# Kernel optimization log

Hardware: AMD Instinct MI355X
Metric: run time of the kernel (lower is better)

The kernel has to match this reference:

```python
import jax, jax.numpy as jnp
import numpy as np

DIM = 768
H = 12
HD = DIM // H  # 64
B = 16
N = 1025  # cls token + 1024 patches; RoPE applied to tokens 1:


def setup_inputs() -> dict:
    key = jax.random.key(0)
    k1, k2, k3, k4, k5, k6 = jax.random.split(key, 6)
    x = jax.random.normal(k1, (B, N, DIM), dtype=jnp.float32)
    # rotary angles for the N-1 non-cls tokens, HD//2 freq pairs
    theta = jax.random.uniform(k2, (N - 1, HD // 2), dtype=jnp.float32) * 2.0 * jnp.pi
    freqs_cos = jnp.cos(theta)
    freqs_sin = jnp.sin(theta)
    W_qkv = jax.random.normal(k3, (3 * DIM, DIM), dtype=jnp.float32) * 0.02
    W_proj = jax.random.normal(k4, (DIM, DIM), dtype=jnp.float32) * 0.02
    b_proj = jax.random.normal(k5, (DIM,), dtype=jnp.float32) * 0.02
    return {"x": x, "freqs_cos": freqs_cos, "freqs_sin": freqs_sin,
            "W_qkv": W_qkv, "W_proj": W_proj, "b_proj": b_proj}


def _apply_rope(t, cos, sin):
    # t: [b, h, m, d]; cos/sin: [m, d/2]. Pairs are interleaved (even, odd),
    # matching torch.view_as_complex on a (..., d/2, 2) reshape.
    tr = t[..., 0::2]
    ti = t[..., 1::2]
    cos = cos[None, None, :, :]
    sin = sin[None, None, :, :]
    out_r = tr * cos - ti * sin
    out_i = tr * sin + ti * cos
    # interleave back: (..., d/2, 2) -> (..., d)
    out = jnp.stack([out_r, out_i], axis=-1)
    return out.reshape(t.shape)


def reference(x, freqs_cos, freqs_sin, W_qkv, W_proj, b_proj):
    b, n, dim = x.shape
    h, hd = H, HD
    scale = hd ** -0.5

    qkv = jnp.einsum('bnd,ed->bne', x, W_qkv)            # [b, n, 3*dim]
    qkv = qkv.reshape(b, n, 3, h, hd)
    q = jnp.transpose(qkv[:, :, 0], (0, 2, 1, 3))         # [b, h, n, hd]
    k = jnp.transpose(qkv[:, :, 1], (0, 2, 1, 3))
    v = jnp.transpose(qkv[:, :, 2], (0, 2, 1, 3))

    # RoPE on all tokens except the cls token (index 0)
    q = jnp.concatenate([q[:, :, :1], _apply_rope(q[:, :, 1:], freqs_cos, freqs_sin)], axis=2)
    k = jnp.concatenate([k[:, :, :1], _apply_rope(k[:, :, 1:], freqs_cos, freqs_sin)], axis=2)

    dots = jnp.einsum('bhid,bhjd->bhij', q, k) * scale    # [b, h, n, n]
    attn = jax.nn.softmax(dots, axis=-1)
    out = jnp.einsum('bhij,bhjd->bhid', attn, v)          # [b, h, n, hd]
    out = jnp.transpose(out, (0, 2, 1, 3)).reshape(b, n, dim)
    out = jnp.einsum('bnd,ed->bne', out, W_proj) + b_proj
    return out
```

## Files before the change

kernel.cpp:

```cpp
#include <hip/hip_runtime.h>
#include <stdint.h>

#define NH 12
#define HD64 64
#define SEQ 1025
#define M_ROWS (16 * SEQ)
#define DIM 768
#define NPAD 1088

typedef __attribute__((ext_vector_type(8))) short bf16x8;
typedef __attribute__((ext_vector_type(4))) float f32x4;
typedef __attribute__((ext_vector_type(4))) short s16x4;

#define VMCNT(n) asm volatile("s_waitcnt vmcnt(" #n ")" ::: "memory")

__device__ __forceinline__ short f2bf_rne(float f) {
    union { float f; uint32_t u; } c; c.f = f;
    uint32_t u = c.u + 0x7fffu + ((c.u >> 16) & 1u);
    return (short)(u >> 16);
}

__device__ __forceinline__ int cvt_pk_bf16(float lo, float hi) {
    int r;
    asm("v_cvt_pk_bf16_f32 %0, %1, %2" : "=v"(r) : "v"(lo), "v"(hi));
    return r;
}

__device__ __forceinline__ void gload_lds16(const void* g, void* l) {
    __builtin_amdgcn_global_load_lds(
        (const __attribute__((address_space(1))) void*)g,
        (__attribute__((address_space(3))) void*)l, 16, 0, 0);
}

__device__ __forceinline__ int xcd_chunk_swizzle(int orig, int nwg) {
    int q = nwg >> 3, r = nwg & 7;
    int xcd = orig & 7, i = orig >> 3;
    int start = (xcd < r) ? xcd * (q + 1) : r * (q + 1) + (xcd - r) * q;
    return start + i;
}

__global__ void f2bf3_kernel(const float* __restrict__ a, short* __restrict__ ao, int na4,
                             const float* __restrict__ b, short* __restrict__ bo, int nb4,
                             const float* __restrict__ c, short* __restrict__ co, int nc4) {
    int i = blockIdx.x * blockDim.x + threadIdx.x;
    const float* src; short* dst; int idx;
    if (i < na4) { src = a; dst = ao; idx = i; }
    else if (i < na4 + nb4) { src = b; dst = bo; idx = i - na4; }
    else if (i < na4 + nb4 + nc4) { src = c; dst = co; idx = i - na4 - nb4; }
    else return;
    f32x4 f = ((const f32x4*)src)[idx];
    s16x4 o;
    o[0] = f2bf_rne(f[0]); o[1] = f2bf_rne(f[1]);
    o[2] = f2bf_rne(f[2]); o[3] = f2bf_rne(f[3]);
    ((s16x4*)dst)[idx] = o;
}


__global__ __launch_bounds__(512) void qkv_gemm_kernel(
    const short* __restrict__ xb, const short* __restrict__ wb,
    const float* __restrict__ fcos, const float* __restrict__ fsin,
    short* __restrict__ Qb, short* __restrict__ Kb, short* __restrict__ VTb)
{
    __shared__ short Alds[4][256 * 32];
    __shared__ short Blds[4][256 * 32];
    const int tid = threadIdx.x;
    const int lane = tid & 63, w = tid >> 6;
    const int wm = w >> 2, wn = w & 3;
    const int lr = lane & 15, lg = lane >> 4;
    const int tile = xcd_chunk_swizzle(blockIdx.x, 65 * 9);
    const int mt = tile / 9, nt = tile - (tile / 9) * 9;

    const int c0 = tid, c1 = tid + 512;
    int ra0 = mt * 256 + (c0 >> 2); if (ra0 > M_ROWS - 1) ra0 = M_ROWS - 1;
    int ra1 = mt * 256 + (c1 >> 2); if (ra1 > M_ROWS - 1) ra1 = M_ROWS - 1;
    const int g0 = (c0 & 3) ^ ((c0 >> 2) & 3) ^ ((c0 >> 4) & 1);
    const int g1 = (c1 & 3) ^ ((c1 >> 2) & 3) ^ ((c1 >> 4) & 1);
    const short* gA0 = xb + (size_t)ra0 * DIM + g0 * 8;
    const short* gA1 = xb + (size_t)ra1 * DIM + g1 * 8;
    const short* gB0 = wb + (size_t)(nt * 256 + (c0 >> 2)) * DIM + g0 * 8;
    const short* gB1 = wb + (size_t)(nt * 256 + (c1 >> 2)) * DIM + g1 * 8;
    short* lA0 = &Alds[0][0] + c0 * 8;
    short* lA1 = &Alds[0][0] + c1 * 8;
    short* lB0 = &Blds[0][0] + c0 * 8;
    short* lB1 = &Blds[0][0] + c1 * 8;

    auto stage = [&](int buf, int kt) {
        const int ko = kt * 32;
        const int lo = buf * (256 * 32);
        gload_lds16(gA0 + ko, lA0 + lo);
        gload_lds16(gA1 + ko, lA1 + lo);
        gload_lds16(gB0 + ko, lB0 + lo);
        gload_lds16(gB1 + ko, lB1 + lo);
    };

    f32x4 acc[8][4];
#pragma unroll
    for (int i = 0; i < 8; i++)
#pragma unroll
        for (int j = 0; j < 4; j++) acc[i][j] = (f32x4)0.0f;

    stage(0, 0); stage(1, 1); stage(2, 2);

    const int ablk = (lg ^ (lr & 3) ^ ((lr >> 2) & 1)) * 8;

    for (int t = 0; t < 24; ++t) {
        if (t < 22) { VMCNT(8); } else if (t == 22) { VMCNT(4); } else { VMCNT(0); }
        __builtin_amdgcn_s_barrier();

        const short* Ab = &Alds[0][0] + (t & 3) * (256 * 32);
        const short* Bb = &Blds[0][0] + (t & 3) * (256 * 32);

        if (t < 21) stage((t + 3) & 3, t + 3);

        bf16x8 bF[4], aF[8];
#pragma unroll
        for (int ni = 0; ni < 4; ni++)
            bF[ni] = *(const bf16x8*)&Bb[(wn * 64 + ni * 16 + lr) * 32 + ablk];
#pragma unroll
        for (int mi = 0; mi < 8; mi++)
            aF[mi] = *(const bf16x8*)&Ab[(wm * 128 + mi * 16 + lr) * 32 + ablk];

        __builtin_amdgcn_s_setprio(1);
#pragma unroll
        for (int mi = 0; mi < 8; mi++)
#pragma unroll
            for (int ni = 0; ni < 4; ni++)
                acc[mi][ni] = __builtin_amdgcn_mfma_f32_16x16x32_bf16(aF[mi], bF[ni], acc[mi][ni], 0, 0, 0);
        __builtin_amdgcn_s_setprio(0);
    }

#pragma unroll
    for (int mi = 0; mi < 8; mi++) {
        int mbase = mt * 256 + wm * 128 + mi * 16 + lg * 4;
#pragma unroll
        for (int j = 0; j < 4; j++) {
            int m = mbase + j;
            bool valid = (m < M_ROWS);
            int mm = valid ? m : 0;
            int b = mm / SEQ;
            int n = mm - b * SEQ;
#pragma unroll
            for (int ni = 0; ni < 4; ni++) {
                int e = nt * 256 + wn * 64 + ni * 16 + lr;
                int qkv = e / DIM;
                int rem = e - qkv * DIM;
                int h = rem >> 6, d = rem & 63;
                float v = acc[mi][ni][j];
                float vo = __shfl_xor(v, 1);
                float outv = v;
                if (qkv < 2 && n > 0) {
                    float cs = fcos[(n - 1) * 32 + (d >> 1)];
                    float sn = fsin[(n - 1) * 32 + (d >> 1)];
                    outv = (d & 1) ? (vo * sn + v * cs) : (v * cs - vo * sn);
                }
                if (qkv == 0) outv *= 0.180336881f;
                if (valid) {
                    short bv = f2bf_rne(outv);
                    size_t bh = (size_t)b * NH + h;
                    if (qkv == 0)      Qb[(bh * SEQ + n) * HD64 + d] = bv;
                    else if (qkv == 1) Kb[(bh * SEQ + n) * HD64 + d] = bv;
                    else               VTb[(bh * HD64 + d) * NPAD + n] = bv;
                }
            }
        }
    }
}

__global__ __launch_bounds__(256) void attn_kernel(
    const short* __restrict__ Qb, const short* __restrict__ Kb,
    const short* __restrict__ VTb, short* __restrict__ AO)
{
    __shared__ short Klds[2][64 * 64];
    __shared__ short Vlds[2][64 * 64];
    __shared__ int Plds[4][16 * 32];
    const int tid = threadIdx.x;
    const int lane = tid & 63, w = tid >> 6;
    const int lr = lane & 15, lg = lane >> 4;
    const int tile = xcd_chunk_swizzle(blockIdx.x, 17 * 192);
    const int bh = tile / 17, qt = tile - (tile / 17) * 17;
    const int b = bh / NH, h = bh - b * NH;

    const short* Qp = Qb + (size_t)bh * SEQ * HD64;
    const short* Kp = Kb + (size_t)bh * SEQ * HD64;
    const short* Vp = VTb + (size_t)bh * HD64 * NPAD;

    int qr = qt * 64 + w * 16 + lr; if (qr > SEQ - 1) qr = SEQ - 1;
    bf16x8 qf0 = *(const bf16x8*)&Qp[(size_t)qr * HD64 + 0 + lg * 8];
    bf16x8 qf1 = *(const bf16x8*)&Qp[(size_t)qr * HD64 + 32 + lg * 8];

    float m_i = -1e30f, l_i = 0.f;
    f32x4 acc[4];
#pragma unroll
    for (int vt = 0; vt < 4; vt++) acc[vt] = (f32x4)0.0f;

    int* pw = &Plds[w][0];
    const int pswz = (lr & 3) << 3;

    auto stageKV = [&](int buf, int t) {
        int k0 = t * 64;
#pragma unroll
        for (int i = 0; i < 2; i++) {
            int c = i * 256 + tid;
            int row = c >> 3, ccd = c & 7;
            int cl = ccd ^ (row & 7);
            int krow = k0 + row; if (krow > SEQ - 1) krow = SEQ - 1;
            gload_lds16(Kp + (size_t)krow * HD64 + cl * 8, &Klds[buf][c * 8]);
            gload_lds16(Vp + (size_t)row * NPAD + k0 + cl * 8, &Vlds[buf][c * 8]);
        }
    };

    stageKV(0, 0);
    asm volatile("s_waitcnt vmcnt(0)" ::: "memory");
    __syncthreads();

    for (int t = 0; t < 17; ++t) {
        int cur = t & 1;
        if (t < 16) stageKV(cur ^ 1, t + 1);

        f32x4 s[4];
        __builtin_amdgcn_s_setprio(1);
#pragma unroll
        for (int k16 = 0; k16 < 4; k16++) {
            int krow = k16 * 16 + lr;
            bf16x8 kf0 = *(const bf16x8*)&Klds[cur][krow * 64 + ((0 + lg) ^ (krow & 7)) * 8];
            bf16x8 kf1 = *(const bf16x8*)&Klds[cur][krow * 64 + ((4 + lg) ^ (krow & 7)) * 8];
            f32x4 d = (f32x4)0.0f;
            d = __builtin_amdgcn_mfma_f32_16x16x32_bf16(kf0, qf0, d, 0, 0, 0);
            d = __builtin_amdgcn_mfma_f32_16x16x32_bf16(kf1, qf1, d, 0, 0, 0);
            s[k16] = d;
        }
        __builtin_amdgcn_s_setprio(0);
        if (t == 16) {
            s[0][0] = (lg == 0) ? s[0][0] : -1e30f;
            s[0][1] = -1e30f; s[0][2] = -1e30f; s[0][3] = -1e30f;
#pragma unroll
            for (int k16 = 1; k16 < 4; k16++) { s[k16][0] = -1e30f; s[k16][1] = -1e30f; s[k16][2] = -1e30f; s[k16][3] = -1e30f; }
        }

        float a0 = fmaxf(s[0][0], s[0][1]), a1 = fmaxf(s[0][2], s[0][3]);
        float a2 = fmaxf(s[1][0], s[1][1]), a3 = fmaxf(s[1][2], s[1][3]);
        float a4 = fmaxf(s[2][0], s[2][1]), a5 = fmaxf(s[2][2], s[2][3]);
        float a6 = fmaxf(s[3][0], s[3][1]), a7 = fmaxf(s[3][2], s[3][3]);
        float b0 = fmaxf(fmaxf(a0, a1), fmaxf(a2, a3));
        float b1 = fmaxf(fmaxf(a4, a5), fmaxf(a6, a7));
        float pmax = fmaxf(b0, b1);
        pmax = fmaxf(pmax, __shfl_xor(pmax, 16));
        pmax = fmaxf(pmax, __shfl_xor(pmax, 32));

        if (__any(pmax > m_i + 11.54f)) {
            float mnew = fmaxf(m_i, pmax);
            float sc = exp2f(m_i - mnew);
            m_i = mnew;
            l_i *= sc;
#pragma unroll
            for (int j = 0; j < 4; j++) {
                float scj = __shfl(sc, 4 * lg + j);
#pragma unroll
                for (int vt = 0; vt < 4; vt++) acc[vt][j] *= scj;
            }
        }

#pragma unroll
        for (int k16 = 0; k16 < 4; k16++) {
#pragma unroll
            for (int j = 0; j < 4; j++) s[k16][j] = exp2f(s[k16][j] - m_i);
        }
        float r0 = (s[0][0] + s[0][1]) + (s[0][2] + s[0][3]);
        float r1 = (s[1][0] + s[1][1]) + (s[1][2] + s[1][3]);
        float r2 = (s[2][0] + s[2][1]) + (s[2][2] + s[2][3]);
        float r3 = (s[3][0] + s[3][1]) + (s[3][2] + s[3][3]);
        float rowsum = (r0 + r1) + (r2 + r3);
        rowsum += __shfl_xor(rowsum, 16);
        rowsum += __shfl_xor(rowsum, 32);
        l_i += rowsum;

#pragma unroll
        for (int k16 = 0; k16 < 4; k16++) {
            int pk0 = cvt_pk_bf16(s[k16][0], s[k16][1]);
            int pk1 = cvt_pk_bf16(s[k16][2], s[k16][3]);
            int pbase = 8 * k16 + 2 * lg;
            pw[lr * 32 + ((pbase + 0) ^ pswz)] = pk0;
            pw[lr * 32 + ((pbase + 1) ^ pswz)] = pk1;
        }
        bf16x8 pa0 = *(const bf16x8*)&pw[lr * 32 + ((4 * lg) ^ pswz)];
        bf16x8 pa1 = *(const bf16x8*)&pw[lr * 32 + ((16 + 4 * lg) ^ pswz)];

        __builtin_amdgcn_s_setprio(1);
#pragma unroll
        for (int vt = 0; vt < 4; vt++) {
            int dr = vt * 16 + lr;
            bf16x8 vf0 = *(const bf16x8*)&Vlds[cur][dr * 64 + ((0 + lg) ^ (dr & 7)) * 8];
            bf16x8 vf1 = *(const bf16x8*)&Vlds[cur][dr * 64 + ((4 + lg) ^ (dr & 7)) * 8];
            acc[vt] = __builtin_amdgcn_mfma_f32_16x16x32_bf16(pa0, vf0, acc[vt], 0, 0, 0);
            acc[vt] = __builtin_amdgcn_mfma_f32_16x16x32_bf16(pa1, vf1, acc[vt], 0, 0, 0);
        }
        __builtin_amdgcn_s_setprio(0);

        asm volatile("s_waitcnt vmcnt(0)" ::: "memory");
        __syncthreads();
    }

    float inv[4];
#pragma unroll
    for (int j = 0; j < 4; j++) inv[j] = 1.0f / __shfl(l_i, 4 * lg + j);
#pragma unroll
    for (int vt = 0; vt < 4; vt++) {
#pragma unroll
        for (int j = 0; j < 4; j++) {
            int qrow = qt * 64 + w * 16 + lg * 4 + j;
            if (qrow < SEQ) {
                AO[((size_t)(b * SEQ + qrow)) * DIM + h * HD64 + vt * 16 + lr] =
                    f2bf_rne(acc[vt][j] * inv[j]);
            }
        }
    }
}

__global__ __launch_bounds__(512) void proj_gemm_kernel(
    const short* __restrict__ ab, const short* __restrict__ wb,
    const float* __restrict__ bias, float* __restrict__ out)
{
    __shared__ short Alds[4][256 * 32];
    __shared__ short Blds[4][256 * 32];
    const int tid = threadIdx.x;
    const int lane = tid & 63, w = tid >> 6;
    const int wm = w >> 2, wn = w & 3;
    const int lr = lane & 15, lg = lane >> 4;
    const int tile = xcd_chunk_swizzle(blockIdx.x, 65 * 3);
    const int mt = tile / 3, nt = tile - (tile / 3) * 3;

    const int c0 = tid, c1 = tid + 512;
    int ra0 = mt * 256 + (c0 >> 2); if (ra0 > M_ROWS - 1) ra0 = M_ROWS - 1;
    int ra1 = mt * 256 + (c1 >> 2); if (ra1 > M_ROWS - 1) ra1 = M_ROWS - 1;
    const int g0 = (c0 & 3) ^ ((c0 >> 2) & 3) ^ ((c0 >> 4) & 1);
    const int g1 = (c1 & 3) ^ ((c1 >> 2) & 3) ^ ((c1 >> 4) & 1);
    const short* gA0 = ab + (size_t)ra0 * DIM + g0 * 8;
    const short* gA1 = ab + (size_t)ra1 * DIM + g1 * 8;
    const short* gB0 = wb + (size_t)(nt * 256 + (c0 >> 2)) * DIM + g0 * 8;
    const short* gB1 = wb + (size_t)(nt * 256 + (c1 >> 2)) * DIM + g1 * 8;
    short* lA0 = &Alds[0][0] + c0 * 8;
    short* lA1 = &Alds[0][0] + c1 * 8;
    short* lB0 = &Blds[0][0] + c0 * 8;
    short* lB1 = &Blds[0][0] + c1 * 8;

    auto stage = [&](int buf, int kt) {
        const int ko = kt * 32;
        const int lo = buf * (256 * 32);
        gload_lds16(gA0 + ko, lA0 + lo);
        gload_lds16(gA1 + ko, lA1 + lo);
        gload_lds16(gB0 + ko, lB0 + lo);
        gload_lds16(gB1 + ko, lB1 + lo);
    };

    f32x4 acc[8][4];
#pragma unroll
    for (int i = 0; i < 8; i++)
#pragma unroll
        for (int j = 0; j < 4; j++) acc[i][j] = (f32x4)0.0f;

    stage(0, 0); stage(1, 1); stage(2, 2);

    const int ablk = (lg ^ (lr & 3) ^ ((lr >> 2) & 1)) * 8;

    for (int t = 0; t < 24; ++t) {
        if (t < 22) { VMCNT(8); } else if (t == 22) { VMCNT(4); } else { VMCNT(0); }
        __builtin_amdgcn_s_barrier();

        const short* Ab = &Alds[0][0] + (t & 3) * (256 * 32);
        const short* Bb = &Blds[0][0] + (t & 3) * (256 * 32);

        if (t < 21) stage((t + 3) & 3, t + 3);

        bf16x8 bF[4], aF[8];
#pragma unroll
        for (int ni = 0; ni < 4; ni++)
            bF[ni] = *(const bf16x8*)&Bb[(wn * 64 + ni * 16 + lr) * 32 + ablk];
#pragma unroll
        for (int mi = 0; mi < 8; mi++)
            aF[mi] = *(const bf16x8*)&Ab[(wm * 128 + mi * 16 + lr) * 32 + ablk];

        __builtin_amdgcn_s_setprio(1);
#pragma unroll
        for (int mi = 0; mi < 8; mi++)
#pragma unroll
            for (int ni = 0; ni < 4; ni++)
                acc[mi][ni] = __builtin_amdgcn_mfma_f32_16x16x32_bf16(aF[mi], bF[ni], acc[mi][ni], 0, 0, 0);
        __builtin_amdgcn_s_setprio(0);
    }

#pragma unroll
    for (int ni = 0; ni < 4; ni++) {
        int e = nt * 256 + wn * 64 + ni * 16 + lr;
        float bv = bias[e];
#pragma unroll
        for (int mi = 0; mi < 8; mi++) {
#pragma unroll
            for (int j = 0; j < 4; j++) {
                int m = mt * 256 + wm * 128 + mi * 16 + lg * 4 + j;
                if (m < M_ROWS) out[(size_t)m * DIM + e] = acc[mi][ni][j] + bv;
            }
        }
    }
}

extern "C" void kernel_launch(void* const* d_in, const int* in_sizes, int n_in,
                              void* d_out, int out_size, void* d_ws, size_t ws_size,
                              hipStream_t stream) {
    const float* x     = (const float*)d_in[0];
    const float* fcos  = (const float*)d_in[1];
    const float* fsin  = (const float*)d_in[2];
    const float* wqkv  = (const float*)d_in[3];
    const float* wproj = (const float*)d_in[4];
    const float* bproj = (const float*)d_in[5];
    float* out = (float*)d_out;

    char* ws = (char*)d_ws;
    size_t off = 0;
    auto salloc = [&](size_t bytes) { void* p = ws + off; off += (bytes + 255) & ~(size_t)255; return p; };
    short* xb     = (short*)salloc((size_t)M_ROWS * DIM * 2);
    short* wqkvb  = (short*)salloc((size_t)2304 * DIM * 2);
    short* wprojb = (short*)salloc((size_t)DIM * DIM * 2);
    short* Qb     = (short*)salloc((size_t)192 * SEQ * HD64 * 2);
    short* Kb     = (short*)salloc((size_t)192 * SEQ * HD64 * 2);
    short* VTb    = (short*)salloc((size_t)192 * HD64 * NPAD * 2);
    short* AO     = (short*)salloc((size_t)M_ROWS * DIM * 2);

    {
        int na4 = M_ROWS * DIM / 4;
        int nb4 = 2304 * DIM / 4;
        int nc4 = DIM * DIM / 4;
        int tot = na4 + nb4 + nc4;
        f2bf3_kernel<<<(tot + 255) / 256, 256, 0, stream>>>(x, xb, na4, wqkv, wqkvb, nb4, wproj, wprojb, nc4);
    }

    qkv_gemm_kernel<<<65 * 9, 512, 0, stream>>>(xb, wqkvb, fcos, fsin, Qb, Kb, VTb);
    attn_kernel<<<17 * 192, 256, 0, stream>>>(Qb, Kb, VTb, AO);
    proj_gemm_kernel<<<65 * 3, 512, 0, stream>>>(AO, wprojb, bproj, out);
}
```

Measured before the change: 379.2 us.

## Restructure QKV and proj GEMM mainloops into double-buffered K=64 phased schedule

Both GEMM kernels move from a 4-deep ring of K=32 stages with one barrier per step to a 2-buffer scheme with K=64 steps. Each step is split into four phases, one per M-half and K-half, and each phase interleaves its LDS reads, async global-to-LDS staging and MFMAs between explicit barriers. The LDS swizzle is simplified and launch bounds now pin one block per CU. The QKV epilogue also hoists the per-tile qkv/head index math out of the inner loop. The aim is better overlap of memory and compute, at the cost of more barriers per step and a shallower prefetch.

```diff
diff --git a/kernel.cpp b/kernel.cpp
--- a/kernel.cpp
+++ b/kernel.cpp
@@ -7,12 +7,14 @@
 #define M_ROWS (16 * SEQ)
 #define DIM 768
 #define NPAD 1088
+#define NT 12
 
 typedef __attribute__((ext_vector_type(8))) short bf16x8;
 typedef __attribute__((ext_vector_type(4))) float f32x4;
 typedef __attribute__((ext_vector_type(4))) short s16x4;
 
 #define VMCNT(n) asm volatile("s_waitcnt vmcnt(" #n ")" ::: "memory")
+#define SBAR     asm volatile("s_barrier" ::: "memory")
 
 __device__ __forceinline__ short f2bf_rne(float f) {
     union { float f; uint32_t u; } c; c.f = f;
@@ -56,42 +58,73 @@
 }
 
 
-__global__ __launch_bounds__(512) void qkv_gemm_kernel(
+#define HALF_SH 8192
+
+#define GEMM_PH(kh, mh, Ab, Bb, DO_B, STG, CNT)                                   \
+        {                                                                          \
+            if (DO_B) {                                                            \
+                _Pragma("unroll")                                                  \
+                for (int ni = 0; ni < 4; ni++)                                     \
+                    b[ni] = *(const bf16x8*)&Bb[(wn * 64 + ni * 16 + lr) * 32 + kbp]; \
+            }                                                                      \
+            _Pragma("unroll")                                                      \
+            for (int mi = 0; mi < 4; mi++)                                         \
+                a[mi] = *(const bf16x8*)&Ab[(wm * 128 + (mh) * 64 + mi * 16 + lr) * 32 + kbp]; \
+            STG;                                                                   \
+            CNT;                                                                   \
+            SBAR;                                                                  \
+            __builtin_amdgcn_s_setprio(1);                                         \
+            _Pragma("unroll")                                                      \
+            for (int mi = 0; mi < 4; mi++)                                         \
+                _Pragma("unroll")                                                  \
+                for (int ni = 0; ni < 4; ni++)                                     \
+                    acc[(mh) * 4 + mi][ni] = __builtin_amdgcn_mfma_f32_16x16x32_bf16( \
+                        a[mi], b[ni], acc[(mh) * 4 + mi][ni], 0, 0, 0);            \
+            __builtin_amdgcn_s_setprio(0);                                         \
+            SBAR;                                                                  \
+        }
+
+__global__ __launch_bounds__(512, 1) void qkv_gemm_kernel(
     const short* __restrict__ xb, const short* __restrict__ wb,
     const float* __restrict__ fcos, const float* __restrict__ fsin,
     short* __restrict__ Qb, short* __restrict__ Kb, short* __restrict__ VTb)
 {
-    __shared__ short Alds[4][256 * 32];
-    __shared__ short Blds[4][256 * 32];
+    __shared__ short L[2 * 2 * 2 * HALF_SH];
     const int tid = threadIdx.x;
     const int lane = tid & 63, w = tid >> 6;
     const int wm = w >> 2, wn = w & 3;
     const int lr = lane & 15, lg = lane >> 4;
     const int tile = xcd_chunk_swizzle(blockIdx.x, 65 * 9);
     const int mt = tile / 9, nt = tile - (tile / 9) * 9;
-
-    const int c0 = tid, c1 = tid + 512;
-    int ra0 = mt * 256 + (c0 >> 2); if (ra0 > M_ROWS - 1) ra0 = M_ROWS - 1;
-    int ra1 = mt * 256 + (c1 >> 2); if (ra1 > M_ROWS - 1) ra1 = M_ROWS - 1;
-    const int g0 = (c0 & 3) ^ ((c0 >> 2) & 3) ^ ((c0 >> 4) & 1);
-    const int g1 = (c1 & 3) ^ ((c1 >> 2) & 3) ^ ((c1 >> 4) & 1);
-    const short* gA0 = xb + (size_t)ra0 * DIM + g0 * 8;
-    const short* gA1 = xb + (size_t)ra1 * DIM + g1 * 8;
-    const short* gB0 = wb + (size_t)(nt * 256 + (c0 >> 2)) * DIM + g0 * 8;
-    const short* gB1 = wb + (size_t)(nt * 256 + (c1 >> 2)) * DIM + g1 * 8;
-    short* lA0 = &Alds[0][0] + c0 * 8;
-    short* lA1 = &Alds[0][0] + c1 * 8;
-    short* lB0 = &Blds[0][0] + c0 * 8;
-    short* lB1 = &Blds[0][0] + c1 * 8;
-
-    auto stage = [&](int buf, int kt) {
-        const int ko = kt * 32;
-        const int lo = buf * (256 * 32);
-        gload_lds16(gA0 + ko, lA0 + lo);
-        gload_lds16(gA1 + ko, lA1 + lo);
-        gload_lds16(gB0 + ko, lB0 + lo);
-        gload_lds16(gB1 + ko, lB1 + lo);
+    const int kbp = (lg ^ ((lr >> 1) & 3)) * 8;
+
+    int s_r[2], s_kb[2];
+#pragma unroll
+    for (int i = 0; i < 2; i++) {
+        int slot = tid + i * 512;
+        s_r[i] = slot >> 2;
+        s_kb[i] = ((slot & 3) ^ ((s_r[i] >> 1) & 3)) * 8;
+    }
+    const short* asrc[2]; const short* bsrc[2];
+#pragma unroll
+    for (int i = 0; i < 2; i++) {
+        int ra = mt * 256 + s_r[i]; if (ra > M_ROWS - 1) ra = M_ROWS - 1;
+        asrc[i] = xb + (size_t)ra * DIM + s_kb[i];
+        bsrc[i] = wb + (size_t)(nt * 256 + s_r[i]) * DIM + s_kb[i];
+    }
+
+    auto stageA = [&](int buf, int kh, int kt) {
+#pragma unroll
+        for (int i = 0; i < 2; i++)
+            gload_lds16(asrc[i] + kt * 64 + kh * 32,
+                        &L[((buf * 2 + 0) * 2 + kh) * HALF_SH + (tid + i * 512) * 8]);
     };
+    auto stageB = [&](int buf, int kh, int kt) {
+#pragma unroll
+        for (int i = 0; i < 2; i++)
+            gload_lds16(bsrc[i] + kt * 64 + kh * 32,
+                        &L[((buf * 2 + 1) * 2 + kh) * HALF_SH + (tid + i * 512) * 8]);
+    };
 
     f32x4 acc[8][4];
 #pragma unroll
@@ -99,36 +132,31 @@
 #pragma unroll
         for (int j = 0; j < 4; j++) acc[i][j] = (f32x4)0.0f;
 
-    stage(0, 0); stage(1, 1); stage(2, 2);
-
-    const int ablk = (lg ^ (lr & 3) ^ ((lr >> 2) & 1)) * 8;
-
-    for (int t = 0; t < 24; ++t) {
-        if (t < 22) { VMCNT(8); } else if (t == 22) { VMCNT(4); } else { VMCNT(0); }
-        __builtin_amdgcn_s_barrier();
-
-        const short* Ab = &Alds[0][0] + (t & 3) * (256 * 32);
-        const short* Bb = &Blds[0][0] + (t & 3) * (256 * 32);
-
-        if (t < 21) stage((t + 3) & 3, t + 3);
-
-        bf16x8 bF[4], aF[8];
-#pragma unroll
-        for (int ni = 0; ni < 4; ni++)
-            bF[ni] = *(const bf16x8*)&Bb[(wn * 64 + ni * 16 + lr) * 32 + ablk];
-#pragma unroll
-        for (int mi = 0; mi < 8; mi++)
-            aF[mi] = *(const bf16x8*)&Ab[(wm * 128 + mi * 16 + lr) * 32 + ablk];
-
-        __builtin_amdgcn_s_setprio(1);
-#pragma unroll
-        for (int mi = 0; mi < 8; mi++)
-#pragma unroll
-            for (int ni = 0; ni < 4; ni++)
-                acc[mi][ni] = __builtin_amdgcn_mfma_f32_16x16x32_bf16(aF[mi], bF[ni], acc[mi][ni], 0, 0, 0);
-        __builtin_amdgcn_s_setprio(0);
-    }
-
+    stageA(0, 0, 0); stageB(0, 0, 0); stageA(0, 1, 0); stageB(0, 1, 0);
+    VMCNT(4);
+    SBAR;
+
+    for (int t = 0; t < NT; ++t) {
+        const int bf = t & 1;
+        const bool st = (t + 1 < NT);
+        const short* Ab0 = &L[((bf * 2 + 0) * 2 + 0) * HALF_SH];
+        const short* Ab1 = &L[((bf * 2 + 0) * 2 + 1) * HALF_SH];
+        const short* Bb0 = &L[((bf * 2 + 1) * 2 + 0) * HALF_SH];
+        const short* Bb1 = &L[((bf * 2 + 1) * 2 + 1) * HALF_SH];
+        bf16x8 a[4], b[4];
+
+        GEMM_PH(0, 0, Ab0, Bb0, true,  if (st) stageA(bf ^ 1, 0, t + 1), ((void)0))
+        GEMM_PH(0, 1, Ab0, Bb0, false, if (st) stageB(bf ^ 1, 0, t + 1),
+                if (st) { VMCNT(4); } else { VMCNT(0); })
+        GEMM_PH(1, 0, Ab1, Bb1, true,  if (st) stageA(bf ^ 1, 1, t + 1), ((void)0))
+        GEMM_PH(1, 1, Ab1, Bb1, false, if (st) stageB(bf ^ 1, 1, t + 1),
+                if (st) { VMCNT(4); })
+    }
+
+    const int ebase = nt * 256 + wn * 64;
+    const int qkvi = ebase / DIM;
+    const int h = (ebase - qkvi * DIM) >> 6;
+    const float qscale = (qkvi == 0) ? 0.180336881f : 1.0f;
 #pragma unroll
     for (int mi = 0; mi < 8; mi++) {
         int mbase = mt * 256 + wm * 128 + mi * 16 + lg * 4;
@@ -137,30 +165,110 @@
             int m = mbase + j;
             bool valid = (m < M_ROWS);
             int mm = valid ? m : 0;
-            int b = mm / SEQ;
-            int n = mm - b * SEQ;
+            int b2 = mm / SEQ;
+            int n = mm - b2 * SEQ;
+            size_t bh = (size_t)b2 * NH + h;
 #pragma unroll
             for (int ni = 0; ni < 4; ni++) {
-                int e = nt * 256 + wn * 64 + ni * 16 + lr;
-                int qkv = e / DIM;
-                int rem = e - qkv * DIM;
-                int h = rem >> 6, d = rem & 63;
+                int d = ni * 16 + lr;
                 float v = acc[mi][ni][j];
                 float vo = __shfl_xor(v, 1);
                 float outv = v;
-                if (qkv < 2 && n > 0) {
-                    float cs = fcos[(n - 1) * 32 + (d >> 1)];
-                    float sn = fsin[(n - 1) * 32 + (d >> 1)];
+                if (qkvi < 2 && n > 0) {
+                    float cs = fcos[(n - 1) * 32 + ni * 8 + (lr >> 1)];
+                    float sn = fsin[(n - 1) * 32 + ni * 8 + (lr >> 1)];
                     outv = (d & 1) ? (vo * sn + v * cs) : (v * cs - vo * sn);
                 }
-                if (qkv == 0) outv *= 0.180336881f;
+                outv *= qscale;
                 if (valid) {
                     short bv = f2bf_rne(outv);
-                    size_t bh = (size_t)b * NH + h;
-                    if (qkv == 0)      Qb[(bh * SEQ + n) * HD64 + d] = bv;
-                    else if (qkv == 1) Kb[(bh * SEQ + n) * HD64 + d] = bv;
-                    else               VTb[(bh * HD64 + d) * NPAD + n] = bv;
+                    if (qkvi == 0)      Qb[(bh * SEQ + n) * HD64 + d] = bv;
+                    else if (qkvi == 1) Kb[(bh * SEQ + n) * HD64 + d] = bv;
+                    else                VTb[(bh * HD64 + d) * NPAD + n] = bv;
                 }
+            }
+        }
+    }
+}
+
+__global__ __launch_bounds__(512, 1) void proj_gemm_kernel(
+    const short* __restrict__ ab, const short* __restrict__ wb,
+    const float* __restrict__ bias, float* __restrict__ out)
+{
+    __shared__ short L[2 * 2 * 2 * HALF_SH];
+    const int tid = threadIdx.x;
+    const int lane = tid & 63, w = tid >> 6;
+    const int wm = w >> 2, wn = w & 3;
+    const int lr = lane & 15, lg = lane >> 4;
+    const int tile = xcd_chunk_swizzle(blockIdx.x, 65 * 3);
+    const int mt = tile / 3, nt = tile - (tile / 3) * 3;
+    const int kbp = (lg ^ ((lr >> 1) & 3)) * 8;
+
+    int s_r[2], s_kb[2];
+#pragma unroll
+    for (int i = 0; i < 2; i++) {
+        int slot = tid + i * 512;
+        s_r[i] = slot >> 2;
+        s_kb[i] = ((slot & 3) ^ ((s_r[i] >> 1) & 3)) * 8;
+    }
+    const short* asrc[2]; const short* bsrc[2];
+#pragma unroll
+    for (int i = 0; i < 2; i++) {
+        int ra = mt * 256 + s_r[i]; if (ra > M_ROWS - 1) ra = M_ROWS - 1;
+        asrc[i] = ab + (size_t)ra * DIM + s_kb[i];
+        bsrc[i] = wb + (size_t)(nt * 256 + s_r[i]) * DIM + s_kb[i];
+    }
+
+    auto stageA = [&](int buf, int kh, int kt) {
+#pragma unroll
+        for (int i = 0; i < 2; i++)
+            gload_lds16(asrc[i] + kt * 64 + kh * 32,
+                        &L[((buf * 2 + 0) * 2 + kh) * HALF_SH + (tid + i * 512) * 8]);
+    };
+    auto stageB = [&](int buf, int kh, int kt) {
+#pragma unroll
+        for (int i = 0; i < 2; i++)
+            gload_lds16(bsrc[i] + kt * 64 + kh * 32,
+                        &L[((buf * 2 + 1) * 2 + kh) * HALF_SH + (tid + i * 512) * 8]);
+    };
+
+    f32x4 acc[8][4];
+#pragma unroll
+    for (int i = 0; i < 8; i++)
+#pragma unroll
+        for (int j = 0; j < 4; j++) acc[i][j] = (f32x4)0.0f;
+
+    stageA(0, 0, 0); stageB(0, 0, 0); stageA(0, 1, 0); stageB(0, 1, 0);
+    VMCNT(4);
+    SBAR;
+
+    for (int t = 0; t < NT; ++t) {
+        const int bf = t & 1;
+        const bool st = (t + 1 < NT);
+        const short* Ab0 = &L[((bf * 2 + 0) * 2 + 0) * HALF_SH];
+        const short* Ab1 = &L[((bf * 2 + 0) * 2 + 1) * HALF_SH];
+        const short* Bb0 = &L[((bf * 2 + 1) * 2 + 0) * HALF_SH];
+        const short* Bb1 = &L[((bf * 2 + 1) * 2 + 1) * HALF_SH];
+        bf16x8 a[4], b[4];
+
+        GEMM_PH(0, 0, Ab0, Bb0, true,  if (st) stageA(bf ^ 1, 0, t + 1), ((void)0))
+        GEMM_PH(0, 1, Ab0, Bb0, false, if (st) stageB(bf ^ 1, 0, t + 1),
+                if (st) { VMCNT(4); } else { VMCNT(0); })
+        GEMM_PH(1, 0, Ab1, Bb1, true,  if (st) stageA(bf ^ 1, 1, t + 1), ((void)0))
+        GEMM_PH(1, 1, Ab1, Bb1, false, if (st) stageB(bf ^ 1, 1, t + 1),
+                if (st) { VMCNT(4); })
+    }
+
+#pragma unroll
+    for (int ni = 0; ni < 4; ni++) {
+        int e = nt * 256 + wn * 64 + ni * 16 + lr;
+        float bv = bias[e];
+#pragma unroll
+        for (int mi = 0; mi < 8; mi++) {
+#pragma unroll
+            for (int j = 0; j < 4; j++) {
+                int m = mt * 256 + wm * 128 + mi * 16 + lg * 4 + j;
+                if (m < M_ROWS) out[(size_t)m * DIM + e] = acc[mi][ni][j] + bv;
             }
         }
     }
@@ -316,93 +424,6 @@
     }
 }
 
-__global__ __launch_bounds__(512) void proj_gemm_kernel(
-    const short* __restrict__ ab, const short* __restrict__ wb,
-    const float* __restrict__ bias, float* __restrict__ out)
-{
-    __shared__ short Alds[4][256 * 32];
-    __shared__ short Blds[4][256 * 32];
-    const int tid = threadIdx.x;
-    const int lane = tid & 63, w = tid >> 6;
-    const int wm = w >> 2, wn = w & 3;
-    const int lr = lane & 15, lg = lane >> 4;
-    const int tile = xcd_chunk_swizzle(blockIdx.x, 65 * 3);
-    const int mt = tile / 3, nt = tile - (tile / 3) * 3;
-
-    const int c0 = tid, c1 = tid + 512;
-    int ra0 = mt * 256 + (c0 >> 2); if (ra0 > M_ROWS - 1) ra0 = M_ROWS - 1;
-    int ra1 = mt * 256 + (c1 >> 2); if (ra1 > M_ROWS - 1) ra1 = M_ROWS - 1;
-    const int g0 = (c0 & 3) ^ ((c0 >> 2) & 3) ^ ((c0 >> 4) & 1);
-    const int g1 = (c1 & 3) ^ ((c1 >> 2) & 3) ^ ((c1 >> 4) & 1);
-    const short* gA0 = ab + (size_t)ra0 * DIM + g0 * 8;
-    const short* gA1 = ab + (size_t)ra1 * DIM + g1 * 8;
-    const short* gB0 = wb + (size_t)(nt * 256 + (c0 >> 2)) * DIM + g0 * 8;
-    const short* gB1 = wb + (size_t)(nt * 256 + (c1 >> 2)) * DIM + g1 * 8;
-    short* lA0 = &Alds[0][0] + c0 * 8;
-    short* lA1 = &Alds[0][0] + c1 * 8;
-    short* lB0 = &Blds[0][0] + c0 * 8;
-    short* lB1 = &Blds[0][0] + c1 * 8;
-
-    auto stage = [&](int buf, int kt) {
-        const int ko = kt * 32;
-        const int lo = buf * (256 * 32);
-        gload_lds16(gA0 + ko, lA0 + lo);
-        gload_lds16(gA1 + ko, lA1 + lo);
-        gload_lds16(gB0 + ko, lB0 + lo);
-        gload_lds16(gB1 + ko, lB1 + lo);
-    };
-
-    f32x4 acc[8][4];
-#pragma unroll
-    for (int i = 0; i < 8; i++)
-#pragma unroll
-        for (int j = 0; j < 4; j++) acc[i][j] = (f32x4)0.0f;
-
-    stage(0, 0); stage(1, 1); stage(2, 2);
-
-    const int ablk = (lg ^ (lr & 3) ^ ((lr >> 2) & 1)) * 8;
-
-    for (int t = 0; t < 24; ++t) {
-        if (t < 22) { VMCNT(8); } else if (t == 22) { VMCNT(4); } else { VMCNT(0); }
-        __builtin_amdgcn_s_barrier();
-
-        const short* Ab = &Alds[0][0] + (t & 3) * (256 * 32);
-        const short* Bb = &Blds[0][0] + (t & 3) * (256 * 32);
-
-        if (t < 21) stage((t + 3) & 3, t + 3);
-
-        bf16x8 bF[4], aF[8];
-#pragma unroll
-        for (int ni = 0; ni < 4; ni++)
-            bF[ni] = *(const bf16x8*)&Bb[(wn * 64 + ni * 16 + lr) * 32 + ablk];
-#pragma unroll
-        for (int mi = 0; mi < 8; mi++)
-            aF[mi] = *(const bf16x8*)&Ab[(wm * 128 + mi * 16 + lr) * 32 + ablk];
-
-        __builtin_amdgcn_s_setprio(1);
-#pragma unroll
-        for (int mi = 0; mi < 8; mi++)
-#pragma unroll
-            for (int ni = 0; ni < 4; ni++)
-                acc[mi][ni] = __builtin_amdgcn_mfma_f32_16x16x32_bf16(aF[mi], bF[ni], acc[mi][ni], 0, 0, 0);
-        __builtin_amdgcn_s_setprio(0);
-    }
-
-#pragma unroll
-    for (int ni = 0; ni < 4; ni++) {
-        int e = nt * 256 + wn * 64 + ni * 16 + lr;
-        float bv = bias[e];
-#pragma unroll
-        for (int mi = 0; mi < 8; mi++) {
-#pragma unroll
-            for (int j = 0; j < 4; j++) {
-                int m = mt * 256 + wm * 128 + mi * 16 + lg * 4 + j;
-                if (m < M_ROWS) out[(size_t)m * DIM + e] = acc[mi][ni][j] + bv;
-            }
-        }
-    }
-}
-
 extern "C" void kernel_launch(void* const* d_in, const int* in_sizes, int n_in,
                               void* d_out, int out_size, void* d_ws, size_t ws_size,
                               hipStream_t stream) {
```

Result: faster. 340.3 us (-10.3%).
